# Optimization experiments

Measured on AMD Instinct MI355X. Metric: run time of the kernel, lower is better.

## Reference

```python
import jax, jax.numpy as jnp
import numpy as np

B, T, D, H, L, FF, SPLIT = 2, 4096, 256, 4 * 0 + 8, 4, 1024, 2048
HD = D // H
EPS = 1e-5


def _layernorm(x, s, b):
    mu = jnp.mean(x, axis=-1, keepdims=True)
    var = jnp.mean(jnp.square(x - mu), axis=-1, keepdims=True)
    return (x - mu) * jax.lax.rsqrt(var + EPS) * s + b


def setup_inputs() -> dict:
    key = jax.random.key(0)
    ks = jax.random.split(key, 10)
    sc = 0.02
    inp = {
        "rows": jax.random.normal(ks[0], (B, T, D), jnp.float32),
        "train_target_embeddings": jax.random.normal(ks[1], (B, SPLIT, D), jnp.float32),
        "Wq": sc * jax.random.normal(ks[2], (L, D, D), jnp.float32),
        "bq": jnp.zeros((L, D), jnp.float32),
        "Wk": sc * jax.random.normal(ks[3], (L, D, D), jnp.float32),
        "bk": jnp.zeros((L, D), jnp.float32),
        "Wv": sc * jax.random.normal(ks[4], (L, D, D), jnp.float32),
        "bv": jnp.zeros((L, D), jnp.float32),
        "Wo": sc * jax.random.normal(ks[5], (L, D, D), jnp.float32),
        "bo": jnp.zeros((L, D), jnp.float32),
        "W1": sc * jax.random.normal(ks[6], (L, D, FF), jnp.float32),
        "b1": jnp.zeros((L, FF), jnp.float32),
        "W2": sc * jax.random.normal(ks[7], (L, FF, D), jnp.float32),
        "b2": jnp.zeros((L, D), jnp.float32),
        "ln1_s": jnp.ones((L, D), jnp.float32),
        "ln1_b": jnp.zeros((L, D), jnp.float32),
        "ln2_s": jnp.ones((L, D), jnp.float32),
        "ln2_b": jnp.zeros((L, D), jnp.float32),
        "split": SPLIT,
    }
    return inp


def reference(rows, train_target_embeddings, Wq, bq, Wk, bk, Wv, bv, Wo, bo,
              W1, b1, W2, b2, ln1_s, ln1_b, ln2_s, ln2_b, split):
    # residual add of train target embeddings onto the train rows
    x = rows.at[:, :split, :].add(train_target_embeddings)
    t = x.shape[1]
    # allowed mask: every query can see all train columns; test queries also see themselves
    key_is_train = jnp.arange(t) < split                      # [T]
    allowed = key_is_train[None, :] | jnp.eye(t, dtype=bool)  # [T,T]
    neg = jnp.asarray(-1e9, x.dtype)
    scale = 1.0 / np.sqrt(HD)
    n_layers = Wq.shape[0]
    for l in range(n_layers):
        # multi-head attention with structured mask
        q = (x @ Wq[l] + bq[l]).reshape(x.shape[0], t, H, HD)
        k = (x @ Wk[l] + bk[l]).reshape(x.shape[0], t, H, HD)
        v = (x @ Wv[l] + bv[l]).reshape(x.shape[0], t, H, HD)
        logits = jnp.einsum('bqhd,bkhd->bhqk', q, k) * scale
        logits = jnp.where(allowed[None, None], logits, neg)
        attn = jax.nn.softmax(logits, axis=-1)
        o = jnp.einsum('bhqk,bkhd->bqhd', attn, v).reshape(x.shape[0], t, D)
        x = _layernorm(x + (o @ Wo[l] + bo[l]), ln1_s[l], ln1_b[l])
        # feed-forward
        h = jax.nn.gelu(x @ W1[l] + b1[l])
        x = _layernorm(x + (h @ W2[l] + b2[l]), ln2_s[l], ln2_b[l])
    return x
```

## Files before the change

### kernel.cpp

```cpp
#include <hip/hip_runtime.h>
#include <cstdint>
#include <cstddef>

#define TSEQ 4096
#define BATCH 2
#define DIM 256
#define NHEAD 8
#define HDIM 32
#define NLAYER 4
#define FFDIM 1024
#define SPLITN 2048
#define MROWS (BATCH * TSEQ)

#define QSCALE 0.2550784545f

typedef __attribute__((ext_vector_type(4))) float f32x4;
typedef __attribute__((ext_vector_type(8))) short bf16x8;

__device__ __forceinline__ short f2bf(float f) {
  union { float f; uint32_t u; } v; v.f = f;
  uint32_t r = v.u + 0x7fffu + ((v.u >> 16) & 1u);
  return (short)(r >> 16);
}

__device__ __forceinline__ float bf2f(short s) {
  union { uint32_t u; float f; } v; v.u = ((uint32_t)(uint16_t)s) << 16;
  return v.f;
}

__device__ __forceinline__ float fast_exp2(float x) {
#if __has_builtin(__builtin_amdgcn_exp2f)
  return __builtin_amdgcn_exp2f(x);
#else
  float r;
  asm volatile("v_exp_f32 %0, %1\n\ts_nop 1" : "=v"(r) : "v"(x));
  return r;
#endif
}

__device__ __forceinline__ uint32_t pack2bf(float a, float b) {
  union { float f; uint32_t u; } ua, ub; ua.f = a; ub.f = b;
  return ((ua.u + 0x8000u) >> 16) | ((ub.u + 0x8000u) & 0xffff0000u);
}

__device__ __forceinline__ float gelu_f(float x) {
  float u = 0.7978845608f * x * (1.0f + 0.044715f * x * x);
  u = fminf(fmaxf(u, -20.f), 20.f);
  float e = fast_exp2(2.885390082f * u);
  float t = (e - 1.0f) / (e + 1.0f);
  return 0.5f * x * (1.0f + t);
}

#define AS1 __attribute__((address_space(1)))
#define AS3 __attribute__((address_space(3)))
__device__ __forceinline__ void gload16(const void* g, void* l) {
  __builtin_amdgcn_global_load_lds((AS1 void*)g, (AS3 void*)l, 16, 0, 0);
}

__global__ __launch_bounds__(256) void prep_w(
    const float* __restrict__ Wq, const float* __restrict__ Wk,
    const float* __restrict__ Wv, const float* __restrict__ Wo,
    const float* __restrict__ W1, const float* __restrict__ W2,
    short* __restrict__ qkvT, short* __restrict__ woT,
    short* __restrict__ w1T, short* __restrict__ w2T)
{
  const int NQKV = NLAYER * 768 * DIM;
  const int NO   = NLAYER * DIM * DIM;
  const int NF   = NLAYER * FFDIM * DIM;
  const int total = NQKV + NO + 2 * NF;
  for (int idx = blockIdx.x * 256 + threadIdx.x; idx < total; idx += gridDim.x * 256) {
    if (idx < NQKV) {
      const int l = idx / (768 * DIM);
      const int rem = idx - l * 768 * DIM;
      const int n = rem >> 8, k = rem & 255;
      const float* src = (n < 256) ? Wq : ((n < 512) ? Wk : Wv);
      qkvT[idx] = f2bf(src[((size_t)l * DIM + k) * DIM + (n & 255)]);
    } else if (idx < NQKV + NO) {
      const int j = idx - NQKV;
      const int l = j >> 16;
      const int rem = j & 65535;
      const int n = rem >> 8, k = rem & 255;
      woT[j] = f2bf(Wo[((size_t)l * DIM + k) * DIM + n]);
    } else if (idx < NQKV + NO + NF) {
      const int j = idx - NQKV - NO;
      const int l = j >> 18;
      const int rem = j & 262143;
      const int n = rem >> 8, k = rem & 255;
      w1T[j] = f2bf(W1[((size_t)l * DIM + k) * FFDIM + n]);
    } else {
      const int j = idx - NQKV - NO - NF;
      const int l = j >> 18;
      const int rem = j & 262143;
      const int n = rem >> 10, k = rem & 1023;
      w2T[j] = f2bf(W2[((size_t)l * FFDIM + k) * DIM + n]);
    }
  }
}

__global__ __launch_bounds__(256) void prep_x(
    const float* __restrict__ rows, const float* __restrict__ tte,
    float* __restrict__ xf, short* __restrict__ xb)
{
  const size_t idx = (size_t)blockIdx.x * 256 + threadIdx.x;
  float4 v = ((const float4*)rows)[idx];
  const size_t e = idx * 4;
  const int m = (int)(e >> 8);
  const int d = (int)(e & 255);
  const int t = m & (TSEQ - 1);
  const int bb = m >> 12;
  if (t < SPLITN) {
    const float4 a = ((const float4*)tte)[((size_t)bb * SPLITN + t) * (DIM / 4) + (d >> 2)];
    v.x += a.x; v.y += a.y; v.z += a.z; v.w += a.w;
  }
  ((float4*)xf)[idx] = v;
  short4 pk; pk.x = f2bf(v.x); pk.y = f2bf(v.y); pk.z = f2bf(v.z); pk.w = f2bf(v.w);
  ((short4*)xb)[idx] = pk;
}

#define GBM 128
#define GBN 64
#define GBK 64

template<int EPI>
__global__ __launch_bounds__(256, 4) void gemm_bt(
    const short* __restrict__ A, const short* __restrict__ BT,
    const float* __restrict__ bias0, const float* __restrict__ bias1,
    const float* __restrict__ bias2, void* __restrict__ Cout,
    int M, int N, int K)
{
  __shared__ short As[GBM * GBK];
  __shared__ short Bs[GBN * GBK];
  const int tid = threadIdx.x;
  const int lane = tid & 63;
  const int wave = tid >> 6;
  const int wm = wave & 1, wn = wave >> 1;
  const int col = lane & 15, quad = lane >> 4;

  const short* Ab = A + (size_t)blockIdx.x * GBM * K;
  const short* Bb = BT + (size_t)blockIdx.y * GBN * K;

  const f32x4 fz = {0.f, 0.f, 0.f, 0.f};
  f32x4 acc[4][2];
#pragma unroll
  for (int i = 0; i < 4; ++i)
#pragma unroll
    for (int j = 0; j < 2; ++j) acc[i][j] = fz;

  for (int k0 = 0; k0 < K; k0 += GBK) {
#pragma unroll
    for (int p = 0; p < 4; ++p) {
      int i = p * 256 + tid;
      gload16(Ab + (size_t)(i >> 3) * K + k0 + (i & 7) * 8, &As[i * 8]);
    }
#pragma unroll
    for (int p = 0; p < 2; ++p) {
      int i = p * 256 + tid;
      gload16(Bb + (size_t)(i >> 3) * K + k0 + (i & 7) * 8, &Bs[i * 8]);
    }
    __syncthreads();
#pragma unroll
    for (int ks = 0; ks < GBK; ks += 32) {
      bf16x8 af[4], bfr[2];
#pragma unroll
      for (int tm = 0; tm < 4; ++tm)
        af[tm] = *(const bf16x8*)&As[(wm * 64 + tm * 16 + col) * GBK + ks + quad * 8];
#pragma unroll
      for (int tn = 0; tn < 2; ++tn)
        bfr[tn] = *(const bf16x8*)&Bs[(wn * 32 + tn * 16 + col) * GBK + ks + quad * 8];
#pragma unroll
      for (int tm = 0; tm < 4; ++tm)
#pragma unroll
        for (int tn = 0; tn < 2; ++tn)
          acc[tm][tn] = __builtin_amdgcn_mfma_f32_16x16x32_bf16(af[tm], bfr[tn], acc[tm][tn], 0, 0, 0);
    }
    __syncthreads();
  }

#pragma unroll
  for (int tm = 0; tm < 4; ++tm) {
    const int mbase = blockIdx.x * GBM + wm * 64 + tm * 16 + quad * 4;
#pragma unroll
    for (int tn = 0; tn < 2; ++tn) {
      const int n = blockIdx.y * GBN + wn * 32 + tn * 16 + col;
      float bv;
      if (EPI == 1) bv = (n < 256) ? bias0[n] : ((n < 512) ? bias1[n - 256] : bias2[n - 512]);
      else          bv = bias0[n];
#pragma unroll
      for (int r = 0; r < 4; ++r) {
        float v = acc[tm][tn][r] + bv;
        size_t off = (size_t)(mbase + r) * N + n;
        if (EPI == 1) {
          if (n < 256) v *= QSCALE;
          ((short*)Cout)[off] = f2bf(v);
        } else {
          ((short*)Cout)[off] = f2bf(gelu_f(v));
        }
      }
    }
  }
}

template<int MODE>
__global__ __launch_bounds__(256, 3) void gemm_ln(
    const short* __restrict__ A, const float* __restrict__ Opart,
    const float* __restrict__ lpart,
    const short* __restrict__ BT, const float* __restrict__ bias,
    const float* __restrict__ xres,
    const float* __restrict__ gs, const float* __restrict__ gb,
    float* __restrict__ xoutf, short* __restrict__ xoutb, int K)
{
  __shared__ short As[32 * 64];
  __shared__ short Bs[256 * 64];
  __shared__ float ssum[4][32], ssq[4][32];
  const int tid = threadIdx.x;
  const int lane = tid & 63;
  const int wave = tid >> 6;
  const int col = lane & 15, quad = lane >> 4;
  const int m0 = blockIdx.x * 32;

  const f32x4 fz = {0.f, 0.f, 0.f, 0.f};
  f32x4 acc[2][4];
#pragma unroll
  for (int i = 0; i < 2; ++i)
#pragma unroll
    for (int j = 0; j < 4; ++j) acc[i][j] = fz;

  const int arow = tid >> 3;
  const int agr  = tid & 7;
  const int grow = m0 + arow;

  for (int k0 = 0; k0 < K; k0 += 64) {
    if (MODE == 0) {
      const bf16x8 av = *(const bf16x8*)(A + (size_t)grow * K + k0 + agr * 8);
      *(bf16x8*)&As[arow * 64 + ((agr ^ (arow & 7)) * 8)] = av;
    } else {
      const int tt = grow & (TSEQ - 1), bb = grow >> 12;
      const int head = (k0 >> 5) + (agr >= 4 ? 1 : 0);
      const size_t lidx = (size_t)(bb * 8 + head) * TSEQ + tt;
      const float l = lpart[lidx] + lpart[(size_t)16 * TSEQ + lidx];
      const float li = 1.0f / l;
      const size_t obase = (size_t)grow * DIM + k0 + agr * 8;
      const float4 a0 = *(const float4*)(Opart + obase);
      const float4 a1 = *(const float4*)(Opart + obase + 4);
      const float4 c0 = *(const float4*)(Opart + (size_t)MROWS * DIM + obase);
      const float4 c1 = *(const float4*)(Opart + (size_t)MROWS * DIM + obase + 4);
      uint4 w;
      w.x = pack2bf((a0.x + c0.x) * li, (a0.y + c0.y) * li);
      w.y = pack2bf((a0.z + c0.z) * li, (a0.w + c0.w) * li);
      w.z = pack2bf((a1.x + c1.x) * li, (a1.y + c1.y) * li);
      w.w = pack2bf((a1.z + c1.z) * li, (a1.w + c1.w) * li);
      *(uint4*)&As[arow * 64 + ((agr ^ (arow & 7)) * 8)] = w;
    }
#pragma unroll
    for (int p = 0; p < 8; ++p) {
      int i = p * 256 + tid;
      gload16(BT + (size_t)(i >> 3) * K + k0 + (i & 7) * 8, &Bs[i * 8]);
    }
    __syncthreads();
#pragma unroll
    for (int ks = 0; ks < 64; ks += 32) {
      bf16x8 af[2], bfr[4];
#pragma unroll
      for (int tm = 0; tm < 2; ++tm) {
        const int row = tm * 16 + col;
        const int g = (ks >> 3) + quad;
        af[tm] = *(const bf16x8*)&As[row * 64 + ((g ^ (row & 7)) * 8)];
      }
#pragma unroll
      for (int tn = 0; tn < 4; ++tn)
        bfr[tn] = *(const bf16x8*)&Bs[(wave * 64 + tn * 16 + col) * 64 + ks + quad * 8];
#pragma unroll
      for (int tm = 0; tm < 2; ++tm)
#pragma unroll
        for (int tn = 0; tn < 4; ++tn)
          acc[tm][tn] = __builtin_amdgcn_mfma_f32_16x16x32_bf16(af[tm], bfr[tn], acc[tm][tn], 0, 0, 0);
    }
    __syncthreads();
  }

  const float* resb = xres + (size_t)m0 * DIM;
#pragma unroll
  for (int tn = 0; tn < 4; ++tn) {
    const int n = wave * 64 + tn * 16 + col;
    const float bv = bias[n];
#pragma unroll
    for (int tm = 0; tm < 2; ++tm)
#pragma unroll
      for (int r = 0; r < 4; ++r) {
        const int row = tm * 16 + quad * 4 + r;
        acc[tm][tn][r] += bv + resb[(size_t)row * DIM + n];
      }
  }

#pragma unroll
  for (int tm = 0; tm < 2; ++tm)
#pragma unroll
    for (int r = 0; r < 4; ++r) {
      float s = 0.f, q = 0.f;
#pragma unroll
      for (int tn = 0; tn < 4; ++tn) { const float v = acc[tm][tn][r]; s += v; q += v * v; }
      s += __shfl_xor(s, 1); q += __shfl_xor(q, 1);
      s += __shfl_xor(s, 2); q += __shfl_xor(q, 2);
      s += __shfl_xor(s, 4); q += __shfl_xor(q, 4);
      s += __shfl_xor(s, 8); q += __shfl_xor(q, 8);
      if (col == 0) { const int row = tm * 16 + quad * 4 + r; ssum[wave][row] = s; ssq[wave][row] = q; }
    }
  __syncthreads();
  if (tid < 32) {
    const float S = ssum[0][tid] + ssum[1][tid] + ssum[2][tid] + ssum[3][tid];
    const float Q = ssq[0][tid] + ssq[1][tid] + ssq[2][tid] + ssq[3][tid];
    const float mu = S * (1.0f / DIM);
    const float var = Q * (1.0f / DIM) - mu * mu;
    ssum[0][tid] = mu;
    ssq[0][tid] = rsqrtf(var + 1e-5f);
  }
  __syncthreads();

#pragma unroll
  for (int tm = 0; tm < 2; ++tm)
#pragma unroll
    for (int tn = 0; tn < 4; ++tn) {
      const int n = wave * 64 + tn * 16 + col;
      const float g = gs[n], bb = gb[n];
#pragma unroll
      for (int r = 0; r < 4; ++r) {
        const int row = tm * 16 + quad * 4 + r;
        const float out = (acc[tm][tn][r] - ssum[0][row]) * ssq[0][row] * g + bb;
        xoutf[(size_t)(m0 + row) * DIM + n] = out;
        xoutb[(size_t)(m0 + row) * DIM + n] = f2bf(out);
      }
    }
}

#define AKT 64
#define KSPL 1024
#define NKT (KSPL / AKT)

__global__ __launch_bounds__(256, 4) void attn_kernel(
    const short* __restrict__ qkv,
    float* __restrict__ Opart, float* __restrict__ lpart)
{
  __shared__ short Kbuf[2][AKT * HDIM];
  __shared__ short Vbuf[2][HDIM * AKT];
  __shared__ short Pall[4][32][72];
  __shared__ float Pdiag[4][16];

  const int tid = threadIdx.x;
  const int lane = tid & 63;
  const int wave = tid >> 6;
  const int col = lane & 15, quad = lane >> 4;
  const int bh = blockIdx.y;
  const int b = bh >> 3, h = bh & 7;
  const int hz = blockIdx.z;
  const int q0 = blockIdx.x * 128 + wave * 32;

  short (*P)[72] = Pall[wave];

  const short* qbase = qkv + (size_t)b * TSEQ * 768 + h * HDIM;
  const short* kbase = qbase + 256;
  const short* vcol  = qbase + 512;

  const short* ksrc = kbase + (size_t)(hz * KSPL + (tid & 63)) * 768 + (tid >> 6) * 8;
  const int vkey = tid & 63, vhg = tid >> 6;
  const int va = vkey >> 3, vb8 = vkey & 7;
  const short* vsrc = vcol + (size_t)(hz * KSPL + vkey) * 768 + vhg * 8;

  const bf16x8 qf0 = *(const bf16x8*)(qbase + (size_t)(q0 + col) * 768 + quad * 8);
  const bf16x8 qf1 = *(const bf16x8*)(qbase + (size_t)(q0 + 16 + col) * 768 + quad * 8);

  bf16x8 ones;
#pragma unroll
  for (int i = 0; i < 8; ++i) ones[i] = (short)0x3F80;

  const f32x4 fz = {0.f, 0.f, 0.f, 0.f};
  f32x4 o[2][2] = {{fz, fz}, {fz, fz}};
  f32x4 lacc[2] = {fz, fz};

  gload16(ksrc, &Kbuf[0][tid * 8]);
  {
    const bf16x8 v0 = *(const bf16x8*)vsrc;
#pragma unroll
    for (int j = 0; j < 8; ++j)
      Vbuf[0][(vhg * 8 + j) * 64 + ((va ^ j) * 8) + vb8] = v0[j];
  }
  bf16x8 vnext = *(const bf16x8*)(vsrc + (size_t)AKT * 768);

  int cur = 0;
  for (int t = 0; t < NKT; ++t) {
    __syncthreads();
    if (t + 1 < NKT) {
      gload16(ksrc + (size_t)(t + 1) * AKT * 768, &Kbuf[1 - cur][tid * 8]);
#pragma unroll
      for (int j = 0; j < 8; ++j)
        Vbuf[1 - cur][(vhg * 8 + j) * 64 + ((va ^ j) * 8) + vb8] = vnext[j];
      if (t + 2 < NKT) vnext = *(const bf16x8*)(vsrc + (size_t)(t + 2) * AKT * 768);
    }
    const short* kb = Kbuf[cur];
    const short* vb = Vbuf[cur];

#pragma unroll
    for (int st = 0; st < 4; ++st) {
      const bf16x8 kf = *(const bf16x8*)&kb[(quad * 64 + st * 16 + col) * 8];
      const f32x4 s0 = __builtin_amdgcn_mfma_f32_16x16x32_bf16(kf, qf0, fz, 0, 0, 0);
      const f32x4 s1 = __builtin_amdgcn_mfma_f32_16x16x32_bf16(kf, qf1, fz, 0, 0, 0);
      uint2 w0, w1;
      w0.x = pack2bf(fast_exp2(s0[0]), fast_exp2(s0[1]));
      w0.y = pack2bf(fast_exp2(s0[2]), fast_exp2(s0[3]));
      w1.x = pack2bf(fast_exp2(s1[0]), fast_exp2(s1[1]));
      w1.y = pack2bf(fast_exp2(s1[2]), fast_exp2(s1[3]));
      *(uint2*)&P[col][st * 16 + quad * 4] = w0;
      *(uint2*)&P[16 + col][st * 16 + quad * 4] = w1;
    }
    asm volatile("s_waitcnt lgkmcnt(0)" ::: "memory");

#pragma unroll
    for (int kh = 0; kh < 2; ++kh) {
      const bf16x8 pf0 = *(const bf16x8*)&P[col][kh * 32 + quad * 8];
      const bf16x8 pf1 = *(const bf16x8*)&P[16 + col][kh * 32 + quad * 8];
#pragma unroll
      for (int hh = 0; hh < 2; ++hh) {
        const int hd = hh * 16 + col;
        const bf16x8 vf = *(const bf16x8*)&vb[hd * AKT + (((kh * 4 + quad) ^ (hd & 7)) * 8)];
        o[0][hh] = __builtin_amdgcn_mfma_f32_16x16x32_bf16(pf0, vf, o[0][hh], 0, 0, 0);
        o[1][hh] = __builtin_amdgcn_mfma_f32_16x16x32_bf16(pf1, vf, o[1][hh], 0, 0, 0);
      }
      lacc[0] = __builtin_amdgcn_mfma_f32_16x16x32_bf16(pf0, ones, lacc[0], 0, 0, 0);
      lacc[1] = __builtin_amdgcn_mfma_f32_16x16x32_bf16(pf1, ones, lacc[1], 0, 0, 0);
    }
    cur ^= 1;
  }

  if (hz == 1 && blockIdx.x >= SPLITN / 128) {
#pragma unroll
    for (int qsub = 0; qsub < 2; ++qsub) {
      const int qd = q0 + qsub * 16;
      const bf16x8 qf = qsub ? qf1 : qf0;
      const bf16x8 kf = *(const bf16x8*)(kbase + (size_t)(qd + col) * 768 + quad * 8);
      const f32x4 sd = __builtin_amdgcn_mfma_f32_16x16x32_bf16(kf, qf, fz, 0, 0, 0);
      float ps = 0.f;
#pragma unroll
      for (int r = 0; r < 4; ++r)
        if (quad * 4 + r == col) ps = fast_exp2(sd[r]);
      if (quad == (col >> 2)) Pdiag[wave][col] = ps;
      asm volatile("s_waitcnt lgkmcnt(0)" ::: "memory");
      const f32x4 pv = *(const f32x4*)&Pdiag[wave][quad * 4];
#pragma unroll
      for (int r = 0; r < 4; ++r) {
        lacc[qsub][r] += pv[r];
        const size_t vrow = (size_t)(qd + quad * 4 + r) * 768;
#pragma unroll
        for (int hh = 0; hh < 2; ++hh)
          o[qsub][hh][r] += pv[r] * bf2f(vcol[vrow + hh * 16 + col]);
      }
      asm volatile("s_waitcnt lgkmcnt(0)" ::: "memory");
    }
  }

  float* Ob = Opart + (size_t)hz * MROWS * DIM;
  float* lb = lpart + (size_t)hz * 16 * TSEQ + (size_t)bh * TSEQ;
#pragma unroll
  for (int qsub = 0; qsub < 2; ++qsub) {
    const f32x4 la = lacc[qsub];
    const int qq = q0 + qsub * 16 + quad * 4;
    const int rowb = b * TSEQ + qq;
#pragma unroll
    for (int r = 0; r < 4; ++r) {
      if (col == 0) lb[qq + r] = la[r];
#pragma unroll
      for (int hh = 0; hh < 2; ++hh)
        Ob[(size_t)(rowb + r) * DIM + h * HDIM + hh * 16 + col] = o[qsub][hh][r];
    }
  }
}

extern "C" void kernel_launch(void* const* d_in, const int* in_sizes, int n_in,
                              void* d_out, int out_size, void* d_ws, size_t ws_size,
                              hipStream_t stream)
{
  const float* rows = (const float*)d_in[0];
  const float* tte  = (const float*)d_in[1];
  const float* Wq = (const float*)d_in[2];  const float* bq = (const float*)d_in[3];
  const float* Wk = (const float*)d_in[4];  const float* bk = (const float*)d_in[5];
  const float* Wv = (const float*)d_in[6];  const float* bv = (const float*)d_in[7];
  const float* Wo = (const float*)d_in[8];  const float* bo = (const float*)d_in[9];
  const float* W1 = (const float*)d_in[10]; const float* b1 = (const float*)d_in[11];
  const float* W2 = (const float*)d_in[12]; const float* b2 = (const float*)d_in[13];
  const float* ln1s = (const float*)d_in[14]; const float* ln1b = (const float*)d_in[15];
  const float* ln2s = (const float*)d_in[16]; const float* ln2b = (const float*)d_in[17];

  char* p = (char*)d_ws;
  float* xf   = (float*)p;  p += (size_t)MROWS * DIM * 4;
  short* xb   = (short*)p;  p += (size_t)MROWS * DIM * 2;
  short* qkv  = (short*)p;  p += (size_t)MROWS * 768 * 2;
  short* hb   = (short*)p;  p += (size_t)MROWS * FFDIM * 2;
  float* Opart = (float*)p; p += (size_t)2 * MROWS * DIM * 4;
  float* lpart = (float*)p; p += (size_t)2 * 16 * TSEQ * 4;
  short* qkvT = (short*)p;  p += (size_t)NLAYER * 768 * DIM * 2;
  short* woT  = (short*)p;  p += (size_t)NLAYER * DIM * DIM * 2;
  short* w1T  = (short*)p;  p += (size_t)NLAYER * FFDIM * DIM * 2;
  short* w2T  = (short*)p;  p += (size_t)NLAYER * DIM * FFDIM * 2;

  prep_w<<<2048, 256, 0, stream>>>(Wq, Wk, Wv, Wo, W1, W2, qkvT, woT, w1T, w2T);
  prep_x<<<MROWS * DIM / 4 / 256, 256, 0, stream>>>(rows, tte, xf, xb);

  for (int l = 0; l < NLAYER; ++l) {
    gemm_bt<1><<<dim3(MROWS / GBM, 768 / GBN), 256, 0, stream>>>(
        xb, qkvT + (size_t)l * 768 * DIM, bq + l * DIM, bk + l * DIM, bv + l * DIM,
        qkv, MROWS, 768, DIM);
    attn_kernel<<<dim3(TSEQ / 128, BATCH * NHEAD, 2), 256, 0, stream>>>(qkv, Opart, lpart);
    gemm_ln<1><<<MROWS / 32, 256, 0, stream>>>(
        nullptr, Opart, lpart, woT + (size_t)l * DIM * DIM, bo + l * DIM, xf,
        ln1s + l * DIM, ln1b + l * DIM, xf, xb, DIM);
    gemm_bt<3><<<dim3(MROWS / GBM, FFDIM / GBN), 256, 0, stream>>>(
        xb, w1T + (size_t)l * FFDIM * DIM, b1 + l * FFDIM, nullptr, nullptr,
        hb, MROWS, FFDIM, DIM);
    float* xo = (l == NLAYER - 1) ? (float*)d_out : xf;
    gemm_ln<0><<<MROWS / 32, 256, 0, stream>>>(
        hb, nullptr, nullptr, w2T + (size_t)l * DIM * FFDIM,
        b2 + l * DIM, xf, ln2s + l * DIM, ln2b + l * DIM, xo, xb, FFDIM);
  }
}
```

Before: 512.4 us.

## Fuse FFN up/down GEMMs into one kernel, retile QKV GEMM, repack V loads

The FFN up-projection, GELU, down-projection and LayerNorm now run in one kernel per 32-row block. The GELU activations stay in shared memory instead of making a round trip through a global bf16 buffer. The QKV GEMM is specialized with 128x128 tiles. In attention, half the threads pack two key rows into 32-bit LDS stores when transposing V. The fused kernel uses about 100KB of LDS at one block per CU, so W1/W2 are re-streamed per 32-row block and occupancy is lower.

```diff
diff --git a/kernel.cpp b/kernel.cpp
--- a/kernel.cpp
+++ b/kernel.cpp
@@ -117,97 +117,76 @@
   ((short4*)xb)[idx] = pk;
 }
 
-#define GBM 128
-#define GBN 64
-#define GBK 64
-
-template<int EPI>
-__global__ __launch_bounds__(256, 4) void gemm_bt(
+__global__ __launch_bounds__(256, 2) void qkv_gemm(
     const short* __restrict__ A, const short* __restrict__ BT,
-    const float* __restrict__ bias0, const float* __restrict__ bias1,
-    const float* __restrict__ bias2, void* __restrict__ Cout,
-    int M, int N, int K)
+    const float* __restrict__ bq, const float* __restrict__ bk,
+    const float* __restrict__ bv, short* __restrict__ Cout)
 {
-  __shared__ short As[GBM * GBK];
-  __shared__ short Bs[GBN * GBK];
+  __shared__ short As[128 * 64];
+  __shared__ short Bs[128 * 64];
   const int tid = threadIdx.x;
   const int lane = tid & 63;
   const int wave = tid >> 6;
   const int wm = wave & 1, wn = wave >> 1;
   const int col = lane & 15, quad = lane >> 4;
 
-  const short* Ab = A + (size_t)blockIdx.x * GBM * K;
-  const short* Bb = BT + (size_t)blockIdx.y * GBN * K;
+  const short* Ab = A + (size_t)blockIdx.x * 128 * DIM;
+  const short* Bb = BT + (size_t)blockIdx.y * 128 * DIM;
 
   const f32x4 fz = {0.f, 0.f, 0.f, 0.f};
-  f32x4 acc[4][2];
+  f32x4 acc[4][4];
 #pragma unroll
   for (int i = 0; i < 4; ++i)
 #pragma unroll
-    for (int j = 0; j < 2; ++j) acc[i][j] = fz;
-
-  for (int k0 = 0; k0 < K; k0 += GBK) {
+    for (int j = 0; j < 4; ++j) acc[i][j] = fz;
+
+  for (int k0 = 0; k0 < DIM; k0 += 64) {
 #pragma unroll
     for (int p = 0; p < 4; ++p) {
       int i = p * 256 + tid;
-      gload16(Ab + (size_t)(i >> 3) * K + k0 + (i & 7) * 8, &As[i * 8]);
-    }
-#pragma unroll
-    for (int p = 0; p < 2; ++p) {
-      int i = p * 256 + tid;
-      gload16(Bb + (size_t)(i >> 3) * K + k0 + (i & 7) * 8, &Bs[i * 8]);
+      gload16(Ab + (size_t)(i >> 3) * DIM + k0 + (i & 7) * 8, &As[i * 8]);
+      gload16(Bb + (size_t)(i >> 3) * DIM + k0 + (i & 7) * 8, &Bs[i * 8]);
     }
     __syncthreads();
 #pragma unroll
-    for (int ks = 0; ks < GBK; ks += 32) {
-      bf16x8 af[4], bfr[2];
+    for (int ks = 0; ks < 64; ks += 32) {
+      bf16x8 af[4], bf[4];
 #pragma unroll
       for (int tm = 0; tm < 4; ++tm)
-        af[tm] = *(const bf16x8*)&As[(wm * 64 + tm * 16 + col) * GBK + ks + quad * 8];
-#pragma unroll
-      for (int tn = 0; tn < 2; ++tn)
-        bfr[tn] = *(const bf16x8*)&Bs[(wn * 32 + tn * 16 + col) * GBK + ks + quad * 8];
+        af[tm] = *(const bf16x8*)&As[(wm * 64 + tm * 16 + col) * 64 + ks + quad * 8];
+#pragma unroll
+      for (int tn = 0; tn < 4; ++tn)
+        bf[tn] = *(const bf16x8*)&Bs[(wn * 64 + tn * 16 + col) * 64 + ks + quad * 8];
 #pragma unroll
       for (int tm = 0; tm < 4; ++tm)
 #pragma unroll
-        for (int tn = 0; tn < 2; ++tn)
-          acc[tm][tn] = __builtin_amdgcn_mfma_f32_16x16x32_bf16(af[tm], bfr[tn], acc[tm][tn], 0, 0, 0);
+        for (int tn = 0; tn < 4; ++tn)
+          acc[tm][tn] = __builtin_amdgcn_mfma_f32_16x16x32_bf16(af[tm], bf[tn], acc[tm][tn], 0, 0, 0);
     }
     __syncthreads();
   }
 
 #pragma unroll
   for (int tm = 0; tm < 4; ++tm) {
-    const int mbase = blockIdx.x * GBM + wm * 64 + tm * 16 + quad * 4;
-#pragma unroll
-    for (int tn = 0; tn < 2; ++tn) {
-      const int n = blockIdx.y * GBN + wn * 32 + tn * 16 + col;
-      float bv;
-      if (EPI == 1) bv = (n < 256) ? bias0[n] : ((n < 512) ? bias1[n - 256] : bias2[n - 512]);
-      else          bv = bias0[n];
-#pragma unroll
-      for (int r = 0; r < 4; ++r) {
-        float v = acc[tm][tn][r] + bv;
-        size_t off = (size_t)(mbase + r) * N + n;
-        if (EPI == 1) {
-          if (n < 256) v *= QSCALE;
-          ((short*)Cout)[off] = f2bf(v);
-        } else {
-          ((short*)Cout)[off] = f2bf(gelu_f(v));
-        }
-      }
-    }
-  }
-}
-
-template<int MODE>
-__global__ __launch_bounds__(256, 3) void gemm_ln(
-    const short* __restrict__ A, const float* __restrict__ Opart,
-    const float* __restrict__ lpart,
+    const int mbase = blockIdx.x * 128 + wm * 64 + tm * 16 + quad * 4;
+#pragma unroll
+    for (int tn = 0; tn < 4; ++tn) {
+      const int n = blockIdx.y * 128 + wn * 64 + tn * 16 + col;
+      const float bvv = (n < 256) ? bq[n] : ((n < 512) ? bk[n - 256] : bv[n - 512]);
+      const float sc = (n < 256) ? QSCALE : 1.0f;
+#pragma unroll
+      for (int r = 0; r < 4; ++r)
+        Cout[(size_t)(mbase + r) * 768 + n] = f2bf((acc[tm][tn][r] + bvv) * sc);
+    }
+  }
+}
+
+__global__ __launch_bounds__(256, 3) void wo_ln(
+    const float* __restrict__ Opart, const float* __restrict__ lpart,
     const short* __restrict__ BT, const float* __restrict__ bias,
     const float* __restrict__ xres,
     const float* __restrict__ gs, const float* __restrict__ gb,
-    float* __restrict__ xoutf, short* __restrict__ xoutb, int K)
+    float* __restrict__ xoutf, short* __restrict__ xoutb)
 {
   __shared__ short As[32 * 64];
   __shared__ short Bs[256 * 64];
@@ -228,13 +207,10 @@
   const int arow = tid >> 3;
   const int agr  = tid & 7;
   const int grow = m0 + arow;
-
-  for (int k0 = 0; k0 < K; k0 += 64) {
-    if (MODE == 0) {
-      const bf16x8 av = *(const bf16x8*)(A + (size_t)grow * K + k0 + agr * 8);
-      *(bf16x8*)&As[arow * 64 + ((agr ^ (arow & 7)) * 8)] = av;
-    } else {
-      const int tt = grow & (TSEQ - 1), bb = grow >> 12;
+  const int tt = grow & (TSEQ - 1), bb = grow >> 12;
+
+  for (int k0 = 0; k0 < DIM; k0 += 64) {
+    {
       const int head = (k0 >> 5) + (agr >= 4 ? 1 : 0);
       const size_t lidx = (size_t)(bb * 8 + head) * TSEQ + tt;
       const float l = lpart[lidx] + lpart[(size_t)16 * TSEQ + lidx];
@@ -254,7 +230,7 @@
 #pragma unroll
     for (int p = 0; p < 8; ++p) {
       int i = p * 256 + tid;
-      gload16(BT + (size_t)(i >> 3) * K + k0 + (i & 7) * 8, &Bs[i * 8]);
+      gload16(BT + (size_t)(i >> 3) * DIM + k0 + (i & 7) * 8, &Bs[i * 8]);
     }
     __syncthreads();
 #pragma unroll
@@ -321,11 +297,172 @@
 #pragma unroll
     for (int tn = 0; tn < 4; ++tn) {
       const int n = wave * 64 + tn * 16 + col;
-      const float g = gs[n], bb = gb[n];
+      const float g = gs[n], bb2 = gb[n];
 #pragma unroll
       for (int r = 0; r < 4; ++r) {
         const int row = tm * 16 + quad * 4 + r;
-        const float out = (acc[tm][tn][r] - ssum[0][row]) * ssq[0][row] * g + bb;
+        const float out = (acc[tm][tn][r] - ssum[0][row]) * ssq[0][row] * g + bb2;
+        xoutf[(size_t)(m0 + row) * DIM + n] = out;
+        xoutb[(size_t)(m0 + row) * DIM + n] = f2bf(out);
+      }
+    }
+}
+
+#define HP 1032
+
+__global__ __launch_bounds__(256, 1) void ff_fused(
+    const short* __restrict__ xbA, const short* __restrict__ w1T,
+    const float* __restrict__ b1, const short* __restrict__ w2T,
+    const float* __restrict__ b2, const float* __restrict__ xres,
+    const float* __restrict__ gs, const float* __restrict__ gb,
+    float* __restrict__ xoutf, short* __restrict__ xoutb)
+{
+  __shared__ short As[32 * 256];
+  __shared__ short Wb[2][64 * 256];
+  __shared__ short Hs[32 * HP];
+  __shared__ float ssum[4][32], ssq[4][32];
+
+  const int tid = threadIdx.x;
+  const int lane = tid & 63;
+  const int wave = tid >> 6;
+  const int col = lane & 15, quad = lane >> 4;
+  const int m0 = blockIdx.x * 32;
+
+#pragma unroll
+  for (int p = 0; p < 4; ++p) {
+    int i = p * 256 + tid;
+    gload16(xbA + (size_t)(m0 + (i >> 5)) * DIM + (i & 31) * 8, &As[i * 8]);
+  }
+#pragma unroll
+  for (int p = 0; p < 8; ++p) {
+    int i = p * 256 + tid;
+    gload16(w1T + (size_t)(i >> 5) * DIM + (i & 31) * 8, &Wb[0][i * 8]);
+  }
+
+  const f32x4 fz = {0.f, 0.f, 0.f, 0.f};
+  bf16x8 af1[2][8];
+
+  for (int nt = 0; nt < 16; ++nt) {
+    __syncthreads();
+    if (nt + 1 < 16) {
+#pragma unroll
+      for (int p = 0; p < 8; ++p) {
+        int i = p * 256 + tid;
+        gload16(w1T + (size_t)((nt + 1) * 64 + (i >> 5)) * DIM + (i & 31) * 8,
+                &Wb[(nt + 1) & 1][i * 8]);
+      }
+    }
+    if (nt == 0) {
+#pragma unroll
+      for (int tm = 0; tm < 2; ++tm)
+#pragma unroll
+        for (int kf = 0; kf < 8; ++kf)
+          af1[tm][kf] = *(const bf16x8*)&As[(tm * 16 + col) * 256 + kf * 32 + quad * 8];
+    }
+    const short* wb = Wb[nt & 1];
+    f32x4 a0 = fz, a1 = fz;
+#pragma unroll
+    for (int kf = 0; kf < 8; ++kf) {
+      const bf16x8 bfv = *(const bf16x8*)&wb[(wave * 16 + col) * 256 + kf * 32 + quad * 8];
+      a0 = __builtin_amdgcn_mfma_f32_16x16x32_bf16(af1[0][kf], bfv, a0, 0, 0, 0);
+      a1 = __builtin_amdgcn_mfma_f32_16x16x32_bf16(af1[1][kf], bfv, a1, 0, 0, 0);
+    }
+    const int n = nt * 64 + wave * 16 + col;
+    const float bv = b1[n];
+#pragma unroll
+    for (int r = 0; r < 4; ++r) {
+      Hs[(quad * 4 + r) * HP + n]        = f2bf(gelu_f(a0[r] + bv));
+      Hs[(16 + quad * 4 + r) * HP + n]   = f2bf(gelu_f(a1[r] + bv));
+    }
+  }
+  __syncthreads();
+
+#pragma unroll
+  for (int p = 0; p < 8; ++p) {
+    int i = p * 256 + tid;
+    gload16(w2T + (size_t)(i >> 3) * FFDIM + (i & 7) * 8, &Wb[0][i * 8]);
+  }
+
+  f32x4 acc[2][4];
+#pragma unroll
+  for (int i = 0; i < 2; ++i)
+#pragma unroll
+    for (int j = 0; j < 4; ++j) acc[i][j] = fz;
+
+  for (int kt = 0; kt < 16; ++kt) {
+    __syncthreads();
+    if (kt + 1 < 16) {
+#pragma unroll
+      for (int p = 0; p < 8; ++p) {
+        int i = p * 256 + tid;
+        gload16(w2T + (size_t)(i >> 3) * FFDIM + (kt + 1) * 64 + (i & 7) * 8,
+                &Wb[(kt + 1) & 1][i * 8]);
+      }
+    }
+    const short* wb = Wb[kt & 1];
+#pragma unroll
+    for (int ks = 0; ks < 2; ++ks) {
+      bf16x8 af[2], bfr[4];
+#pragma unroll
+      for (int tm = 0; tm < 2; ++tm)
+        af[tm] = *(const bf16x8*)&Hs[(tm * 16 + col) * HP + kt * 64 + ks * 32 + quad * 8];
+#pragma unroll
+      for (int tn = 0; tn < 4; ++tn)
+        bfr[tn] = *(const bf16x8*)&wb[(wave * 64 + tn * 16 + col) * 64 + ks * 32 + quad * 8];
+#pragma unroll
+      for (int tm = 0; tm < 2; ++tm)
+#pragma unroll
+        for (int tn = 0; tn < 4; ++tn)
+          acc[tm][tn] = __builtin_amdgcn_mfma_f32_16x16x32_bf16(af[tm], bfr[tn], acc[tm][tn], 0, 0, 0);
+    }
+  }
+
+  const float* resb = xres + (size_t)m0 * DIM;
+#pragma unroll
+  for (int tn = 0; tn < 4; ++tn) {
+    const int n = wave * 64 + tn * 16 + col;
+    const float bv = b2[n];
+#pragma unroll
+    for (int tm = 0; tm < 2; ++tm)
+#pragma unroll
+      for (int r = 0; r < 4; ++r) {
+        const int row = tm * 16 + quad * 4 + r;
+        acc[tm][tn][r] += bv + resb[(size_t)row * DIM + n];
+      }
+  }
+#pragma unroll
+  for (int tm = 0; tm < 2; ++tm)
+#pragma unroll
+    for (int r = 0; r < 4; ++r) {
+      float s = 0.f, q = 0.f;
+#pragma unroll
+      for (int tn = 0; tn < 4; ++tn) { const float v = acc[tm][tn][r]; s += v; q += v * v; }
+      s += __shfl_xor(s, 1); q += __shfl_xor(q, 1);
+      s += __shfl_xor(s, 2); q += __shfl_xor(q, 2);
+      s += __shfl_xor(s, 4); q += __shfl_xor(q, 4);
+      s += __shfl_xor(s, 8); q += __shfl_xor(q, 8);
+      if (col == 0) { const int row = tm * 16 + quad * 4 + r; ssum[wave][row] = s; ssq[wave][row] = q; }
+    }
+  __syncthreads();
+  if (tid < 32) {
+    const float S = ssum[0][tid] + ssum[1][tid] + ssum[2][tid] + ssum[3][tid];
+    const float Q = ssq[0][tid] + ssq[1][tid] + ssq[2][tid] + ssq[3][tid];
+    const float mu = S * (1.0f / DIM);
+    const float var = Q * (1.0f / DIM) - mu * mu;
+    ssum[0][tid] = mu;
+    ssq[0][tid] = rsqrtf(var + 1e-5f);
+  }
+  __syncthreads();
+#pragma unroll
+  for (int tm = 0; tm < 2; ++tm)
+#pragma unroll
+    for (int tn = 0; tn < 4; ++tn) {
+      const int n = wave * 64 + tn * 16 + col;
+      const float g = gs[n], bb2 = gb[n];
+#pragma unroll
+      for (int r = 0; r < 4; ++r) {
+        const int row = tm * 16 + quad * 4 + r;
+        const float out = (acc[tm][tn][r] - ssum[0][row]) * ssq[0][row] * g + bb2;
         xoutf[(size_t)(m0 + row) * DIM + n] = out;
         xoutb[(size_t)(m0 + row) * DIM + n] = f2bf(out);
       }
@@ -361,9 +498,11 @@
   const short* vcol  = qbase + 512;
 
   const short* ksrc = kbase + (size_t)(hz * KSPL + (tid & 63)) * 768 + (tid >> 6) * 8;
-  const int vkey = tid & 63, vhg = tid >> 6;
-  const int va = vkey >> 3, vb8 = vkey & 7;
-  const short* vsrc = vcol + (size_t)(hz * KSPL + vkey) * 768 + vhg * 8;
+
+  const int vhg = (tid & 127) >> 5, vpr = tid & 31;
+  const int vva = vpr >> 2, vb8 = (vpr & 3) * 2;
+  const short* vsrc = vcol + (size_t)(hz * KSPL + 2 * vpr) * 768 + vhg * 8;
+  const bool vact = (tid < 128);
 
   const bf16x8 qf0 = *(const bf16x8*)(qbase + (size_t)(q0 + col) * 768 + quad * 8);
   const bf16x8 qf1 = *(const bf16x8*)(qbase + (size_t)(q0 + 16 + col) * 768 + quad * 8);
@@ -377,23 +516,35 @@
   f32x4 lacc[2] = {fz, fz};
 
   gload16(ksrc, &Kbuf[0][tid * 8]);
-  {
+  bf16x8 vn0, vn1;
+  if (vact) {
     const bf16x8 v0 = *(const bf16x8*)vsrc;
-#pragma unroll
-    for (int j = 0; j < 8; ++j)
-      Vbuf[0][(vhg * 8 + j) * 64 + ((va ^ j) * 8) + vb8] = v0[j];
-  }
-  bf16x8 vnext = *(const bf16x8*)(vsrc + (size_t)AKT * 768);
+    const bf16x8 v1 = *(const bf16x8*)(vsrc + 768);
+#pragma unroll
+    for (int j = 0; j < 8; ++j) {
+      const uint32_t w = (uint32_t)(uint16_t)v0[j] | ((uint32_t)(uint16_t)v1[j] << 16);
+      *(uint32_t*)&Vbuf[0][(vhg * 8 + j) * 64 + ((vva ^ j) * 8) + vb8] = w;
+    }
+    vn0 = *(const bf16x8*)(vsrc + (size_t)AKT * 768);
+    vn1 = *(const bf16x8*)(vsrc + (size_t)AKT * 768 + 768);
+  }
 
   int cur = 0;
   for (int t = 0; t < NKT; ++t) {
     __syncthreads();
     if (t + 1 < NKT) {
       gload16(ksrc + (size_t)(t + 1) * AKT * 768, &Kbuf[1 - cur][tid * 8]);
-#pragma unroll
-      for (int j = 0; j < 8; ++j)
-        Vbuf[1 - cur][(vhg * 8 + j) * 64 + ((va ^ j) * 8) + vb8] = vnext[j];
-      if (t + 2 < NKT) vnext = *(const bf16x8*)(vsrc + (size_t)(t + 2) * AKT * 768);
+      if (vact) {
+#pragma unroll
+        for (int j = 0; j < 8; ++j) {
+          const uint32_t w = (uint32_t)(uint16_t)vn0[j] | ((uint32_t)(uint16_t)vn1[j] << 16);
+          *(uint32_t*)&Vbuf[1 - cur][(vhg * 8 + j) * 64 + ((vva ^ j) * 8) + vb8] = w;
+        }
+        if (t + 2 < NKT) {
+          vn0 = *(const bf16x8*)(vsrc + (size_t)(t + 2) * AKT * 768);
+          vn1 = *(const bf16x8*)(vsrc + (size_t)(t + 2) * AKT * 768 + 768);
+        }
+      }
     }
     const short* kb = Kbuf[cur];
     const short* vb = Vbuf[cur];
@@ -492,7 +643,6 @@
   float* xf   = (float*)p;  p += (size_t)MROWS * DIM * 4;
   short* xb   = (short*)p;  p += (size_t)MROWS * DIM * 2;
   short* qkv  = (short*)p;  p += (size_t)MROWS * 768 * 2;
-  short* hb   = (short*)p;  p += (size_t)MROWS * FFDIM * 2;
   float* Opart = (float*)p; p += (size_t)2 * MROWS * DIM * 4;
   float* lpart = (float*)p; p += (size_t)2 * 16 * TSEQ * 4;
   short* qkvT = (short*)p;  p += (size_t)NLAYER * 768 * DIM * 2;
@@ -504,19 +654,16 @@
   prep_x<<<MROWS * DIM / 4 / 256, 256, 0, stream>>>(rows, tte, xf, xb);
 
   for (int l = 0; l < NLAYER; ++l) {
-    gemm_bt<1><<<dim3(MROWS / GBM, 768 / GBN), 256, 0, stream>>>(
-        xb, qkvT + (size_t)l * 768 * DIM, bq + l * DIM, bk + l * DIM, bv + l * DIM,
-        qkv, MROWS, 768, DIM);
+    qkv_gemm<<<dim3(MROWS / 128, 6), 256, 0, stream>>>(
+        xb, qkvT + (size_t)l * 768 * DIM, bq + l * DIM, bk + l * DIM, bv + l * DIM, qkv);
     attn_kernel<<<dim3(TSEQ / 128, BATCH * NHEAD, 2), 256, 0, stream>>>(qkv, Opart, lpart);
-    gemm_ln<1><<<MROWS / 32, 256, 0, stream>>>(
-        nullptr, Opart, lpart, woT + (size_t)l * DIM * DIM, bo + l * DIM, xf,
-        ln1s + l * DIM, ln1b + l * DIM, xf, xb, DIM);
-    gemm_bt<3><<<dim3(MROWS / GBM, FFDIM / GBN), 256, 0, stream>>>(
-        xb, w1T + (size_t)l * FFDIM * DIM, b1 + l * FFDIM, nullptr, nullptr,
-        hb, MROWS, FFDIM, DIM);
+    wo_ln<<<MROWS / 32, 256, 0, stream>>>(
+        Opart, lpart, woT + (size_t)l * DIM * DIM, bo + l * DIM, xf,
+        ln1s + l * DIM, ln1b + l * DIM, xf, xb);
     float* xo = (l == NLAYER - 1) ? (float*)d_out : xf;
-    gemm_ln<0><<<MROWS / 32, 256, 0, stream>>>(
-        hb, nullptr, nullptr, w2T + (size_t)l * DIM * FFDIM,
-        b2 + l * DIM, xf, ln2s + l * DIM, ln2b + l * DIM, xo, xb, FFDIM);
-  }
-}
+    ff_fused<<<MROWS / 32, 256, 0, stream>>>(
+        xb, w1T + (size_t)l * FFDIM * DIM, b1 + l * FFDIM,
+        w2T + (size_t)l * DIM * FFDIM, b2 + l * DIM, xf,
+        ln2s + l * DIM, ln2b + l * DIM, xo, xb);
+  }
+}
```

Result: slower. 545.5 us (+6.5%).
